# Optimization experiments

Measured on AMD Instinct MI355X. Metric: run time of the kernel, lower is better.

## Reference

```python
import jax, jax.numpy as jnp
import numpy as np

N, T, DYN, STAT, H = 50000, 24, 16, 8, 64
E = 1_600_000


def gru_last(x, Wih, Whh, bih, bhh):
    # x: [N, T, DYN]; torch GRU gate order: r, z, n
    gx = jnp.einsum('ntd,gd->ntg', x, Wih) + bih  # [N, T, 3H]
    h0 = jnp.zeros((x.shape[0], H), x.dtype)

    def step(h, gx_t):
        gh = h @ Whh.T + bhh  # [N, 3H]
        xr, xz, xn = jnp.split(gx_t, 3, axis=-1)
        hr, hz, hn = jnp.split(gh, 3, axis=-1)
        r = jax.nn.sigmoid(xr + hr)
        z = jax.nn.sigmoid(xz + hz)
        n = jnp.tanh(xn + r * hn)
        h_new = (1.0 - z) * n + z * h
        return h_new, None

    h_last, _ = jax.lax.scan(step, h0, jnp.swapaxes(gx, 0, 1))  # scan over T
    return h_last  # [N, H]


def gcn_layer(x, W, b, src, dst, w):
    h = x @ W  # [N, out]
    msg = h[src] * w[:, None]  # gather + weight  [E, out]
    agg = jax.ops.segment_sum(msg, dst, num_segments=N)  # scatter-add
    return agg + b


def setup_inputs() -> dict:
    key = jax.random.key(0)
    ks = jax.random.split(key, 16)
    s = 0.1
    return {
        'x_dyn': jax.random.normal(ks[0], (N, T, DYN), jnp.float32),
        'x_stat': jax.random.normal(ks[1], (N, STAT), jnp.float32),
        'edge_index': jax.random.randint(ks[2], (2, E), 0, N, jnp.int32),
        'edge_weight': jax.random.uniform(ks[3], (E,), jnp.float32),
        'Wih': jax.random.normal(ks[4], (3 * H, DYN), jnp.float32) * s,
        'Whh': jax.random.normal(ks[5], (3 * H, H), jnp.float32) * s,
        'bih': jnp.zeros((3 * H,), jnp.float32),
        'bhh': jnp.zeros((3 * H,), jnp.float32),
        'W1': jax.random.normal(ks[6], (H + STAT, H), jnp.float32) * s,
        'b1': jnp.zeros((H,), jnp.float32),
        'W2': jax.random.normal(ks[7], (H, H), jnp.float32) * s,
        'b2': jnp.zeros((H,), jnp.float32),
        'Wa': jax.random.normal(ks[8], (H, 1), jnp.float32) * s,
        'ba': jnp.zeros((1,), jnp.float32),
        'Wp': jax.random.normal(ks[9], (H, 1), jnp.float32) * s,
        'bp': jnp.zeros((1,), jnp.float32),
    }


def reference(x_dyn, x_stat, edge_index, edge_weight,
              Wih, Whh, bih, bhh, W1, b1, W2, b2, Wa, ba, Wp, bp):
    src, dst = edge_index[0], edge_index[1]
    z = gru_last(x_dyn, Wih, Whh, bih, bhh)            # [N, H]
    h = jnp.concatenate([z, x_stat], axis=1)           # [N, H+STAT]
    h = jax.nn.relu(gcn_layer(h, W1, b1, src, dst, edge_weight))
    h = jax.nn.relu(gcn_layer(h, W2, b2, src, dst, edge_weight))
    # dropout omitted (eval mode)
    aqi = (h @ Wa + ba)[:, 0]
    pm = (h @ Wp + bp)[:, 0]
    return aqi, pm
```

## Files before the change

### kernel.cpp

```cpp
#include <hip/hip_runtime.h>
#include <cstdint>
#include <cstddef>

#define NNODES 50000
#define TT 24
#define DYNF 16
#define STATF 8
#define HDIM 64
#define NEDGES 1600000
#define NB 32
#define GRU_BLOCKS ((NNODES + NB - 1) / NB)
#define FILL_CHUNK 1024
#define FILL_CHUNKS ((NEDGES + FILL_CHUNK - 1) / FILL_CHUNK)
#define CAP 80

typedef __attribute__((ext_vector_type(8))) short bf16x8;
typedef __attribute__((ext_vector_type(4))) float f32x4;
typedef __attribute__((ext_vector_type(2))) float f32x2;

__device__ __forceinline__ unsigned short f2bf(float f) {
    unsigned u = __float_as_uint(f);
    u = (u + 0x7FFFu + ((u >> 16) & 1u)) >> 16;
    return (unsigned short)u;
}
__device__ __forceinline__ float bf2f(unsigned short s) {
    return __uint_as_float((unsigned)s << 16);
}
__device__ __forceinline__ bf16x8 cvt8(const float* __restrict__ p) {
    bf16x8 r;
    #pragma unroll
    for (int i = 0; i < 8; ++i) r[i] = (short)f2bf(p[i]);
    return r;
}
__device__ __forceinline__ bf16x8 zero8() {
    bf16x8 z;
    #pragma unroll
    for (int i = 0; i < 8; ++i) z[i] = 0;
    return z;
}
__device__ __forceinline__ float fast_tanh(float x) {
    float e = __expf(2.f * x);
    return 1.f - 2.f * __builtin_amdgcn_rcpf(e + 1.f);
}

__global__ __launch_bounds__(256, 4) void gru_fill_kernel(
    const float* __restrict__ x_dyn, const float* __restrict__ x_stat,
    const float* __restrict__ Wih, const float* __restrict__ Whh,
    const float* __restrict__ bih, const float* __restrict__ bhh,
    const float* __restrict__ W1, unsigned short* __restrict__ t1,
    const int* __restrict__ srcv, const int* __restrict__ dstv,
    const float* __restrict__ ew, int* __restrict__ cursor,
    unsigned* __restrict__ csr)
{
    constexpr int S_H = 72;
    constexpr int S_X = 40;
    __shared__ short hbuf[2][NB * S_H];
    __shared__ short xbuf[2][NB * S_X];

    const int tid = (int)threadIdx.x;

    if ((int)blockIdx.x >= GRU_BLOCKS) {
        const int fb = (int)blockIdx.x - GRU_BLOCKS;
        const int range = fb & 7;
        const int chunk = fb >> 3;
        const int base = chunk * FILL_CHUNK;
        const int lo = range * (NNODES / 8);
        const int hi = (range == 7) ? NNODES : lo + (NNODES / 8);
        #pragma unroll
        for (int j = 0; j < FILL_CHUNK / 256; ++j) {
            const int e = base + j * 256 + tid;
            if (e < NEDGES) {
                const int d = dstv[e];
                if (d >= lo && d < hi) {
                    const int s = __builtin_nontemporal_load(srcv + e);
                    const float we = __builtin_nontemporal_load(ew + e);
                    const int pos = atomicAdd(&cursor[d], 1);
                    if (pos < CAP)
                        csr[(size_t)d * CAP + pos] =
                            (unsigned)s | ((unsigned)f2bf(we) << 16);
                }
            }
        }
        return;
    }

    const int lane = tid & 63;
    const int w = __builtin_amdgcn_readfirstlane(tid >> 6);
    const int col = lane & 15;
    const int quad = lane >> 4;
    const int node0 = (int)blockIdx.x * NB;

    bf16x8 Bh[3][2];
    bf16x8 Bx[3];
    #pragma unroll
    for (int g = 0; g < 3; ++g) {
        const int n = (w + g * 4) * 16 + col;
        #pragma unroll
        for (int kt = 0; kt < 2; ++kt)
            Bh[g][kt] = cvt8(Whh + (size_t)n * HDIM + kt * 32 + quad * 8);
        Bx[g] = (quad < 2) ? cvt8(Wih + (size_t)n * DYNF + quad * 8) : zero8();
    }

    const int jg = w * 16 + col;
    const float b_r  = bih[jg]        + bhh[jg];
    const float b_z  = bih[HDIM + jg] + bhh[HDIM + jg];
    const float b_xn = bih[2 * HDIM + jg];
    const float b_hn = bhh[2 * HDIM + jg];

    for (int i = tid; i < NB * S_H; i += 256) hbuf[0][i] = 0;

    auto stage_x = [&](int t, int b) {
        const int nd = tid >> 3, c = tid & 7;
        int node = node0 + nd;
        if (node >= NNODES) node = 0;
        const f32x2 v = __builtin_nontemporal_load(
            reinterpret_cast<const f32x2*>(
                x_dyn + (size_t)node * (TT * DYNF) + t * DYNF + c * 2));
        unsigned pk = (unsigned)f2bf(v[0]) | ((unsigned)f2bf(v[1]) << 16);
        *reinterpret_cast<unsigned*>(&xbuf[b][nd * S_X + c * 2]) = pk;
        *reinterpret_cast<unsigned*>(&xbuf[b][nd * S_X + 16 + c * 2]) = 0u;
    };
    stage_x(0, 0);

    float hprev[2][4];
    #pragma unroll
    for (int mt = 0; mt < 2; ++mt)
        #pragma unroll
        for (int r = 0; r < 4; ++r) hprev[mt][r] = 0.f;

    for (int t = 0; t < TT; ++t) {
        const int rb = t & 1;
        __syncthreads();

        f32x4 accr[2], accz[2], accnh[2], accnx[2];
        #pragma unroll
        for (int mt = 0; mt < 2; ++mt) {
            const int nd = mt * 16 + col;
            const bf16x8 a0 = *reinterpret_cast<const bf16x8*>(&hbuf[rb][nd * S_H + quad * 8]);
            const bf16x8 a1 = *reinterpret_cast<const bf16x8*>(&hbuf[rb][nd * S_H + 32 + quad * 8]);
            const bf16x8 ax = *reinterpret_cast<const bf16x8*>(&xbuf[rb][nd * S_X + quad * 8]);
            const f32x4 z4 = {0.f, 0.f, 0.f, 0.f};
            accr[mt]  = __builtin_amdgcn_mfma_f32_16x16x32_bf16(a0, Bh[0][0], z4, 0, 0, 0);
            accr[mt]  = __builtin_amdgcn_mfma_f32_16x16x32_bf16(a1, Bh[0][1], accr[mt], 0, 0, 0);
            accr[mt]  = __builtin_amdgcn_mfma_f32_16x16x32_bf16(ax, Bx[0],    accr[mt], 0, 0, 0);
            accz[mt]  = __builtin_amdgcn_mfma_f32_16x16x32_bf16(a0, Bh[1][0], z4, 0, 0, 0);
            accz[mt]  = __builtin_amdgcn_mfma_f32_16x16x32_bf16(a1, Bh[1][1], accz[mt], 0, 0, 0);
            accz[mt]  = __builtin_amdgcn_mfma_f32_16x16x32_bf16(ax, Bx[1],    accz[mt], 0, 0, 0);
            accnh[mt] = __builtin_amdgcn_mfma_f32_16x16x32_bf16(a0, Bh[2][0], z4, 0, 0, 0);
            accnh[mt] = __builtin_amdgcn_mfma_f32_16x16x32_bf16(a1, Bh[2][1], accnh[mt], 0, 0, 0);
            accnx[mt] = __builtin_amdgcn_mfma_f32_16x16x32_bf16(ax, Bx[2],    z4, 0, 0, 0);
        }

        if (t + 1 < TT) stage_x(t + 1, rb ^ 1);

        #pragma unroll
        for (int mt = 0; mt < 2; ++mt) {
            #pragma unroll
            for (int r = 0; r < 4; ++r) {
                const float dr = 1.f + __expf(-(accr[mt][r] + b_r));
                const float dz = 1.f + __expf(-(accz[mt][r] + b_z));
                const float q  = __builtin_amdgcn_rcpf(dr * dz);
                const float R  = q * dz;
                const float Z  = q * dr;
                const float Nn = fast_tanh(accnx[mt][r] + b_xn + R * (accnh[mt][r] + b_hn));
                const float hn = Nn + Z * (hprev[mt][r] - Nn);
                hprev[mt][r] = hn;
                hbuf[rb ^ 1][(mt * 16 + quad * 4 + r) * S_H + jg] = (short)f2bf(hn);
            }
        }
    }
    __syncthreads();

    bf16x8 Bw0, Bw1, Bw2;
    #pragma unroll
    for (int j = 0; j < 8; ++j) {
        Bw0[j] = (short)f2bf(W1[(size_t)(quad * 8 + j) * HDIM + jg]);
        Bw1[j] = (short)f2bf(W1[(size_t)(32 + quad * 8 + j) * HDIM + jg]);
    }
    if (quad == 0) {
        #pragma unroll
        for (int j = 0; j < 8; ++j)
            Bw2[j] = (short)f2bf(W1[(size_t)(HDIM + j) * HDIM + jg]);
    } else {
        Bw2 = zero8();
    }

    #pragma unroll
    for (int mt = 0; mt < 2; ++mt) {
        const int nd = mt * 16 + col;
        const bf16x8 a0 = *reinterpret_cast<const bf16x8*>(&hbuf[0][nd * S_H + quad * 8]);
        const bf16x8 a1 = *reinterpret_cast<const bf16x8*>(&hbuf[0][nd * S_H + 32 + quad * 8]);
        bf16x8 axs;
        if (quad == 0) {
            int node = node0 + nd;
            if (node >= NNODES) node = 0;
            axs = cvt8(x_stat + (size_t)node * STATF);
        } else {
            axs = zero8();
        }
        const f32x4 z4 = {0.f, 0.f, 0.f, 0.f};
        f32x4 aw;
        aw = __builtin_amdgcn_mfma_f32_16x16x32_bf16(a0, Bw0, z4, 0, 0, 0);
        aw = __builtin_amdgcn_mfma_f32_16x16x32_bf16(a1, Bw1, aw, 0, 0, 0);
        aw = __builtin_amdgcn_mfma_f32_16x16x32_bf16(axs, Bw2, aw, 0, 0, 0);
        #pragma unroll
        for (int r = 0; r < 4; ++r) {
            const int node = node0 + mt * 16 + quad * 4 + r;
            if (node < NNODES) t1[(size_t)node * HDIM + jg] = f2bf(aw[r]);
        }
    }
}

__global__ __launch_bounds__(256) void gather_transform_kernel(
    const unsigned short* __restrict__ tsrc, const int* __restrict__ cursor,
    const unsigned* __restrict__ csr, const float* __restrict__ b1,
    const float* __restrict__ W2, unsigned short* __restrict__ out)
{
    __shared__ float aggL[16][68];
    const int tid  = (int)threadIdx.x;
    const int lane = tid & 63;
    const int w    = tid >> 6;
    const int half = lane >> 5;
    const int fl   = lane & 31;
    const int col  = lane & 15;
    const int quad = lane >> 4;
    const int node0 = (int)blockIdx.x * 16;
    const int jg = w * 16 + col;

    bf16x8 Bw0, Bw1;
    float bk0[8], bk1[8];
    #pragma unroll
    for (int j = 0; j < 8; ++j) {
        Bw0[j] = (short)f2bf(W2[(size_t)(quad * 8 + j) * HDIM + jg]);
        Bw1[j] = (short)f2bf(W2[(size_t)(32 + quad * 8 + j) * HDIM + jg]);
        bk0[j] = b1[quad * 8 + j];
        bk1[j] = b1[32 + quad * 8 + j];
    }

    for (int i = 0; i < 4; ++i) {
        const int nloc = w * 4 + i;
        const int node = node0 + nloc;
        const int beg = node * CAP;
        const int cnt = min(cursor[node], CAP);
        const int end = beg + cnt;
        float ax = 0.f, ay = 0.f;
        int p = beg;
        for (; p + 8 <= end; p += 8) {
            unsigned pp[4], pk[4];
            #pragma unroll
            for (int k = 0; k < 4; ++k) pp[k] = csr[p + 2 * k + half];
            #pragma unroll
            for (int k = 0; k < 4; ++k)
                pk[k] = *reinterpret_cast<const unsigned*>(
                    tsrc + (size_t)(pp[k] & 0xFFFFu) * HDIM + 2 * fl);
            #pragma unroll
            for (int k = 0; k < 4; ++k) {
                const float wgt = __uint_as_float(pp[k] & 0xFFFF0000u);
                ax += wgt * bf2f((unsigned short)(pk[k] & 0xFFFFu));
                ay += wgt * bf2f((unsigned short)(pk[k] >> 16));
            }
        }
        for (; p + 2 <= end; p += 2) {
            const unsigned pp = csr[p + half];
            const unsigned pk = *reinterpret_cast<const unsigned*>(
                tsrc + (size_t)(pp & 0xFFFFu) * HDIM + 2 * fl);
            const float wgt = __uint_as_float(pp & 0xFFFF0000u);
            ax += wgt * bf2f((unsigned short)(pk & 0xFFFFu));
            ay += wgt * bf2f((unsigned short)(pk >> 16));
        }
        if (p < end) {
            const unsigned pp = csr[p];
            const unsigned pk = *reinterpret_cast<const unsigned*>(
                tsrc + (size_t)(pp & 0xFFFFu) * HDIM + 2 * fl);
            const float wgt = (half == 0) ? __uint_as_float(pp & 0xFFFF0000u) : 0.f;
            ax += wgt * bf2f((unsigned short)(pk & 0xFFFFu));
            ay += wgt * bf2f((unsigned short)(pk >> 16));
        }
        ax += __shfl_xor(ax, 32, 64);
        ay += __shfl_xor(ay, 32, 64);
        if (half == 0) {
            f32x2 o; o[0] = ax; o[1] = ay;
            *reinterpret_cast<f32x2*>(&aggL[nloc][2 * fl]) = o;
        }
    }
    __syncthreads();

    bf16x8 a0, a1;
    #pragma unroll
    for (int j = 0; j < 8; ++j) {
        a0[j] = (short)f2bf(fmaxf(aggL[col][quad * 8 + j] + bk0[j], 0.f));
        a1[j] = (short)f2bf(fmaxf(aggL[col][32 + quad * 8 + j] + bk1[j], 0.f));
    }
    const f32x4 z4 = {0.f, 0.f, 0.f, 0.f};
    f32x4 aw;
    aw = __builtin_amdgcn_mfma_f32_16x16x32_bf16(a0, Bw0, z4, 0, 0, 0);
    aw = __builtin_amdgcn_mfma_f32_16x16x32_bf16(a1, Bw1, aw, 0, 0, 0);
    #pragma unroll
    for (int r = 0; r < 4; ++r)
        out[(size_t)(node0 + quad * 4 + r) * HDIM + jg] = f2bf(aw[r]);
}

__global__ __launch_bounds__(256) void gather_head_kernel(
    const unsigned short* __restrict__ tsrc, const int* __restrict__ cursor,
    const unsigned* __restrict__ csr,
    const float* __restrict__ b2, const float* __restrict__ Wa,
    const float* __restrict__ ba, const float* __restrict__ Wp,
    const float* __restrict__ bp, float* __restrict__ out)
{
    const int node = blockIdx.x * 4 + (threadIdx.x >> 6);
    const int lane = (int)threadIdx.x & 63;
    const int half = lane >> 5;
    const int fl = lane & 31;
    if (node >= NNODES) return;
    const int beg = node * CAP;
    const int cnt = min(cursor[node], CAP);
    const int end = beg + cnt;
    float ax = 0.f, ay = 0.f;
    int i = beg;
    for (; i + 8 <= end; i += 8) {
        unsigned p[4], pk[4];
        #pragma unroll
        for (int k = 0; k < 4; ++k) p[k] = csr[i + 2 * k + half];
        #pragma unroll
        for (int k = 0; k < 4; ++k)
            pk[k] = *reinterpret_cast<const unsigned*>(
                tsrc + (size_t)(p[k] & 0xFFFFu) * HDIM + 2 * fl);
        #pragma unroll
        for (int k = 0; k < 4; ++k) {
            const float wgt = __uint_as_float(p[k] & 0xFFFF0000u);
            ax += wgt * bf2f((unsigned short)(pk[k] & 0xFFFFu));
            ay += wgt * bf2f((unsigned short)(pk[k] >> 16));
        }
    }
    for (; i + 2 <= end; i += 2) {
        const unsigned p = csr[i + half];
        const unsigned pk = *reinterpret_cast<const unsigned*>(
            tsrc + (size_t)(p & 0xFFFFu) * HDIM + 2 * fl);
        const float wgt = __uint_as_float(p & 0xFFFF0000u);
        ax += wgt * bf2f((unsigned short)(pk & 0xFFFFu));
        ay += wgt * bf2f((unsigned short)(pk >> 16));
    }
    if (i < end) {
        const unsigned p = csr[i];
        const unsigned pk = *reinterpret_cast<const unsigned*>(
            tsrc + (size_t)(p & 0xFFFFu) * HDIM + 2 * fl);
        const float wgt = (half == 0) ? __uint_as_float(p & 0xFFFF0000u) : 0.f;
        ax += wgt * bf2f((unsigned short)(pk & 0xFFFFu));
        ay += wgt * bf2f((unsigned short)(pk >> 16));
    }
    ax += __shfl_xor(ax, 32, 64);
    ay += __shfl_xor(ay, 32, 64);

    const float2 bb = *reinterpret_cast<const float2*>(b2 + 2 * fl);
    const float2 wa = *reinterpret_cast<const float2*>(Wa + 2 * fl);
    const float2 wp = *reinterpret_cast<const float2*>(Wp + 2 * fl);
    const float h0 = fmaxf(ax + bb.x, 0.f);
    const float h1 = fmaxf(ay + bb.y, 0.f);
    float sa = h0 * wa.x + h1 * wa.y;
    float sp = h0 * wp.x + h1 * wp.y;
    #pragma unroll
    for (int off = 1; off < 32; off <<= 1) {
        sa += __shfl_xor(sa, off, 64);
        sp += __shfl_xor(sp, off, 64);
    }
    if (lane == 0) {
        out[node] = sa + ba[0];
        out[NNODES + node] = sp + bp[0];
    }
}

extern "C" void kernel_launch(void* const* d_in, const int* in_sizes, int n_in,
                              void* d_out, int out_size, void* d_ws, size_t ws_size,
                              hipStream_t stream)
{
    const float* x_dyn  = (const float*)d_in[0];
    const float* x_stat = (const float*)d_in[1];
    const int*   eidx   = (const int*)  d_in[2];
    const float* ew     = (const float*)d_in[3];
    const float* Wih    = (const float*)d_in[4];
    const float* Whh    = (const float*)d_in[5];
    const float* bih    = (const float*)d_in[6];
    const float* bhh    = (const float*)d_in[7];
    const float* W1     = (const float*)d_in[8];
    const float* b1     = (const float*)d_in[9];
    const float* W2     = (const float*)d_in[10];
    const float* b2     = (const float*)d_in[11];
    const float* Wa     = (const float*)d_in[12];
    const float* ba     = (const float*)d_in[13];
    const float* Wp     = (const float*)d_in[14];
    const float* bp     = (const float*)d_in[15];

    const int* srcv = eidx;
    const int* dstv = eidx + NEDGES;

    const size_t NH = (size_t)NNODES * HDIM;
    float* ws   = (float*)d_ws;
    unsigned short* t1 = (unsigned short*)ws;
    unsigned short* t2 = (unsigned short*)(ws + NH / 2);
    unsigned* csr = (unsigned*)(ws + NH);
    int* cursor = (int*)(csr + (size_t)NNODES * CAP);

    dim3 blk(256);

    hipMemsetAsync(cursor, 0, (size_t)NNODES * sizeof(int), stream);

    gru_fill_kernel<<<dim3(GRU_BLOCKS + FILL_CHUNKS * 8), blk, 0, stream>>>(
        x_dyn, x_stat, Wih, Whh, bih, bhh, W1, t1,
        srcv, dstv, ew, cursor, csr);

    gather_transform_kernel<<<dim3(NNODES / 16), blk, 0, stream>>>(
        t1, cursor, csr, b1, W2, t2);

    gather_head_kernel<<<dim3((NNODES + 3) / 4), blk, 0, stream>>>(
        t2, cursor, csr, b2, Wa, ba, Wp, bp, (float*)d_out);
}
```

Measured before the change: 381.7 us.

## Restructure GRU so each wave owns 16 nodes with no block-level barriers

The GRU recurrence is reorganised so each wavefront handles 16 nodes end to end. Weights sit in the MFMA A operand, all 64 hidden features are computed per wave, and the hidden state goes through a private swizzled LDS slice, so the per-timestep __syncthreads is gone. Biases are folded into the input MFMA through a constant-one column, and x is prefetched straight from global into registers. This trades far more register-resident weights (launch bounds lowered to 2) for less barrier and LDS traffic and more independent MFMA work per wave.

```diff
diff --git a/kernel.cpp b/kernel.cpp
--- a/kernel.cpp
+++ b/kernel.cpp
@@ -8,8 +8,7 @@
 #define STATF 8
 #define HDIM 64
 #define NEDGES 1600000
-#define NB 32
-#define GRU_BLOCKS ((NNODES + NB - 1) / NB)
+#define GRUB 782
 #define FILL_CHUNK 1024
 #define FILL_CHUNKS ((NEDGES + FILL_CHUNK - 1) / FILL_CHUNK)
 #define CAP 80
@@ -17,6 +16,7 @@
 typedef __attribute__((ext_vector_type(8))) short bf16x8;
 typedef __attribute__((ext_vector_type(4))) float f32x4;
 typedef __attribute__((ext_vector_type(2))) float f32x2;
+typedef __attribute__((ext_vector_type(2))) unsigned u32x2;
 
 __device__ __forceinline__ unsigned short f2bf(float f) {
     unsigned u = __float_as_uint(f);
@@ -43,7 +43,7 @@
     return 1.f - 2.f * __builtin_amdgcn_rcpf(e + 1.f);
 }
 
-__global__ __launch_bounds__(256, 4) void gru_fill_kernel(
+__global__ __launch_bounds__(256, 2) void gru_fill_kernel(
     const float* __restrict__ x_dyn, const float* __restrict__ x_stat,
     const float* __restrict__ Wih, const float* __restrict__ Whh,
     const float* __restrict__ bih, const float* __restrict__ bhh,
@@ -52,15 +52,12 @@
     const float* __restrict__ ew, int* __restrict__ cursor,
     unsigned* __restrict__ csr)
 {
-    constexpr int S_H = 72;
-    constexpr int S_X = 40;
-    __shared__ short hbuf[2][NB * S_H];
-    __shared__ short xbuf[2][NB * S_X];
+    __shared__ short hsc[4][1024];
 
     const int tid = (int)threadIdx.x;
 
-    if ((int)blockIdx.x >= GRU_BLOCKS) {
-        const int fb = (int)blockIdx.x - GRU_BLOCKS;
+    if ((int)blockIdx.x >= GRUB) {
+        const int fb = (int)blockIdx.x - GRUB;
         const int range = fb & 7;
         const int chunk = fb >> 3;
         const int base = chunk * FILL_CHUNK;
@@ -85,129 +82,163 @@
     }
 
     const int lane = tid & 63;
-    const int w = __builtin_amdgcn_readfirstlane(tid >> 6);
+    const int wv = tid >> 6;
     const int col = lane & 15;
     const int quad = lane >> 4;
-    const int node0 = (int)blockIdx.x * NB;
-
-    bf16x8 Bh[3][2];
-    bf16x8 Bx[3];
+
+    int node0 = (int)blockIdx.x * 64 + wv * 16;
+    const bool active = node0 < NNODES;
+    if (!active) node0 = 0;
+
+    bf16x8 Wh[3][4][2];
+    bf16x8 Wx[3][4];
     #pragma unroll
     for (int g = 0; g < 3; ++g) {
-        const int n = (w + g * 4) * 16 + col;
-        #pragma unroll
-        for (int kt = 0; kt < 2; ++kt)
-            Bh[g][kt] = cvt8(Whh + (size_t)n * HDIM + kt * 32 + quad * 8);
-        Bx[g] = (quad < 2) ? cvt8(Wih + (size_t)n * DYNF + quad * 8) : zero8();
-    }
-
-    const int jg = w * 16 + col;
-    const float b_r  = bih[jg]        + bhh[jg];
-    const float b_z  = bih[HDIM + jg] + bhh[HDIM + jg];
-    const float b_xn = bih[2 * HDIM + jg];
-    const float b_hn = bhh[2 * HDIM + jg];
-
-    for (int i = tid; i < NB * S_H; i += 256) hbuf[0][i] = 0;
-
-    auto stage_x = [&](int t, int b) {
-        const int nd = tid >> 3, c = tid & 7;
-        int node = node0 + nd;
-        if (node >= NNODES) node = 0;
-        const f32x2 v = __builtin_nontemporal_load(
-            reinterpret_cast<const f32x2*>(
-                x_dyn + (size_t)node * (TT * DYNF) + t * DYNF + c * 2));
-        unsigned pk = (unsigned)f2bf(v[0]) | ((unsigned)f2bf(v[1]) << 16);
-        *reinterpret_cast<unsigned*>(&xbuf[b][nd * S_X + c * 2]) = pk;
-        *reinterpret_cast<unsigned*>(&xbuf[b][nd * S_X + 16 + c * 2]) = 0u;
+        #pragma unroll
+        for (int ft = 0; ft < 4; ++ft) {
+            const int row = g * 64 + ft * 16 + col;
+            Wh[g][ft][0] = cvt8(Whh + (size_t)row * HDIM + quad * 8);
+            Wh[g][ft][1] = cvt8(Whh + (size_t)row * HDIM + 32 + quad * 8);
+            if (quad < 2) {
+                Wx[g][ft] = cvt8(Wih + (size_t)row * DYNF + quad * 8);
+            } else {
+                bf16x8 z = zero8();
+                if (quad == 2) {
+                    const float bias = bih[row] + ((g < 2) ? bhh[row] : 0.f);
+                    z[0] = (short)f2bf(bias);
+                }
+                Wx[g][ft] = z;
+            }
+        }
+    }
+    float bhn[4][4];
+    #pragma unroll
+    for (int ft = 0; ft < 4; ++ft)
+        #pragma unroll
+        for (int r = 0; r < 4; ++r)
+            bhn[ft][r] = bhh[128 + ft * 16 + quad * 4 + r];
+
+    short* hs = &hsc[wv][0];
+    const int wsw = (col & 7) << 3;
+
+    auto xload = [&](int t, f32x4& lo, f32x4& hi) {
+        if (quad < 2) {
+            const float* p = x_dyn + (size_t)(node0 + col) * (TT * DYNF)
+                           + t * DYNF + quad * 8;
+            lo = *reinterpret_cast<const f32x4*>(p);
+            hi = *reinterpret_cast<const f32x4*>(p + 4);
+        }
     };
-    stage_x(0, 0);
-
-    float hprev[2][4];
-    #pragma unroll
-    for (int mt = 0; mt < 2; ++mt)
-        #pragma unroll
-        for (int r = 0; r < 4; ++r) hprev[mt][r] = 0.f;
+    auto xcvt = [&](f32x4 lo, f32x4 hi) -> bf16x8 {
+        bf16x8 b;
+        if (quad < 2) {
+            #pragma unroll
+            for (int i = 0; i < 4; ++i) {
+                b[i] = (short)f2bf(lo[i]);
+                b[4 + i] = (short)f2bf(hi[i]);
+            }
+        } else {
+            b = zero8();
+            if (quad == 2) b[0] = (short)0x3F80;
+        }
+        return b;
+    };
+
+    f32x4 xlo, xhi;
+    xload(0, xlo, xhi);
+    bf16x8 Bh0 = zero8(), Bh1 = zero8();
+    bf16x8 Bx = xcvt(xlo, xhi);
+
+    float hprev[4][4];
+    #pragma unroll
+    for (int ft = 0; ft < 4; ++ft)
+        #pragma unroll
+        for (int r = 0; r < 4; ++r) hprev[ft][r] = 0.f;
+
+    const f32x4 z4 = {0.f, 0.f, 0.f, 0.f};
 
     for (int t = 0; t < TT; ++t) {
-        const int rb = t & 1;
-        __syncthreads();
-
-        f32x4 accr[2], accz[2], accnh[2], accnx[2];
-        #pragma unroll
-        for (int mt = 0; mt < 2; ++mt) {
-            const int nd = mt * 16 + col;
-            const bf16x8 a0 = *reinterpret_cast<const bf16x8*>(&hbuf[rb][nd * S_H + quad * 8]);
-            const bf16x8 a1 = *reinterpret_cast<const bf16x8*>(&hbuf[rb][nd * S_H + 32 + quad * 8]);
-            const bf16x8 ax = *reinterpret_cast<const bf16x8*>(&xbuf[rb][nd * S_X + quad * 8]);
-            const f32x4 z4 = {0.f, 0.f, 0.f, 0.f};
-            accr[mt]  = __builtin_amdgcn_mfma_f32_16x16x32_bf16(a0, Bh[0][0], z4, 0, 0, 0);
-            accr[mt]  = __builtin_amdgcn_mfma_f32_16x16x32_bf16(a1, Bh[0][1], accr[mt], 0, 0, 0);
-            accr[mt]  = __builtin_amdgcn_mfma_f32_16x16x32_bf16(ax, Bx[0],    accr[mt], 0, 0, 0);
-            accz[mt]  = __builtin_amdgcn_mfma_f32_16x16x32_bf16(a0, Bh[1][0], z4, 0, 0, 0);
-            accz[mt]  = __builtin_amdgcn_mfma_f32_16x16x32_bf16(a1, Bh[1][1], accz[mt], 0, 0, 0);
-            accz[mt]  = __builtin_amdgcn_mfma_f32_16x16x32_bf16(ax, Bx[1],    accz[mt], 0, 0, 0);
-            accnh[mt] = __builtin_amdgcn_mfma_f32_16x16x32_bf16(a0, Bh[2][0], z4, 0, 0, 0);
-            accnh[mt] = __builtin_amdgcn_mfma_f32_16x16x32_bf16(a1, Bh[2][1], accnh[mt], 0, 0, 0);
-            accnx[mt] = __builtin_amdgcn_mfma_f32_16x16x32_bf16(ax, Bx[2],    z4, 0, 0, 0);
-        }
-
-        if (t + 1 < TT) stage_x(t + 1, rb ^ 1);
-
-        #pragma unroll
-        for (int mt = 0; mt < 2; ++mt) {
+        f32x4 nlo, nhi;
+        if (t + 1 < TT) xload(t + 1, nlo, nhi);
+
+        #pragma unroll
+        for (int ft = 0; ft < 4; ++ft) {
+            f32x4 ar, az, anh, anx;
+            ar  = __builtin_amdgcn_mfma_f32_16x16x32_bf16(Wh[0][ft][0], Bh0, z4, 0, 0, 0);
+            ar  = __builtin_amdgcn_mfma_f32_16x16x32_bf16(Wh[0][ft][1], Bh1, ar, 0, 0, 0);
+            ar  = __builtin_amdgcn_mfma_f32_16x16x32_bf16(Wx[0][ft],    Bx,  ar, 0, 0, 0);
+            az  = __builtin_amdgcn_mfma_f32_16x16x32_bf16(Wh[1][ft][0], Bh0, z4, 0, 0, 0);
+            az  = __builtin_amdgcn_mfma_f32_16x16x32_bf16(Wh[1][ft][1], Bh1, az, 0, 0, 0);
+            az  = __builtin_amdgcn_mfma_f32_16x16x32_bf16(Wx[1][ft],    Bx,  az, 0, 0, 0);
+            anh = __builtin_amdgcn_mfma_f32_16x16x32_bf16(Wh[2][ft][0], Bh0, z4, 0, 0, 0);
+            anh = __builtin_amdgcn_mfma_f32_16x16x32_bf16(Wh[2][ft][1], Bh1, anh, 0, 0, 0);
+            anx = __builtin_amdgcn_mfma_f32_16x16x32_bf16(Wx[2][ft],    Bx,  z4, 0, 0, 0);
+
+            unsigned plo, phi;
             #pragma unroll
             for (int r = 0; r < 4; ++r) {
-                const float dr = 1.f + __expf(-(accr[mt][r] + b_r));
-                const float dz = 1.f + __expf(-(accz[mt][r] + b_z));
+                const float dr = 1.f + __expf(-ar[r]);
+                const float dz = 1.f + __expf(-az[r]);
                 const float q  = __builtin_amdgcn_rcpf(dr * dz);
                 const float R  = q * dz;
                 const float Z  = q * dr;
-                const float Nn = fast_tanh(accnx[mt][r] + b_xn + R * (accnh[mt][r] + b_hn));
-                const float hn = Nn + Z * (hprev[mt][r] - Nn);
-                hprev[mt][r] = hn;
-                hbuf[rb ^ 1][(mt * 16 + quad * 4 + r) * S_H + jg] = (short)f2bf(hn);
+                const float Nn = fast_tanh(anx[r] + R * (anh[r] + bhn[ft][r]));
+                const float hn = Nn + Z * (hprev[ft][r] - Nn);
+                hprev[ft][r] = hn;
+                const unsigned hb = f2bf(hn);
+                if (r == 0) plo = hb;
+                else if (r == 1) plo |= hb << 16;
+                else if (r == 2) phi = hb;
+                else phi |= hb << 16;
             }
-        }
-    }
-    __syncthreads();
-
-    bf16x8 Bw0, Bw1, Bw2;
-    #pragma unroll
-    for (int j = 0; j < 8; ++j) {
-        Bw0[j] = (short)f2bf(W1[(size_t)(quad * 8 + j) * HDIM + jg]);
-        Bw1[j] = (short)f2bf(W1[(size_t)(32 + quad * 8 + j) * HDIM + jg]);
-    }
-    if (quad == 0) {
-        #pragma unroll
-        for (int j = 0; j < 8; ++j)
-            Bw2[j] = (short)f2bf(W1[(size_t)(HDIM + j) * HDIM + jg]);
-    } else {
-        Bw2 = zero8();
-    }
-
-    #pragma unroll
-    for (int mt = 0; mt < 2; ++mt) {
-        const int nd = mt * 16 + col;
-        const bf16x8 a0 = *reinterpret_cast<const bf16x8*>(&hbuf[0][nd * S_H + quad * 8]);
-        const bf16x8 a1 = *reinterpret_cast<const bf16x8*>(&hbuf[0][nd * S_H + 32 + quad * 8]);
-        bf16x8 axs;
+            u32x2 pk; pk[0] = plo; pk[1] = phi;
+            *reinterpret_cast<u32x2*>(
+                &hs[col * 64 + ((ft * 16 + quad * 4) ^ wsw)]) = pk;
+        }
+
+        Bh0 = *reinterpret_cast<const bf16x8*>(&hs[col * 64 + ((quad * 8) ^ wsw)]);
+        Bh1 = *reinterpret_cast<const bf16x8*>(&hs[col * 64 + ((32 + quad * 8) ^ wsw)]);
+        if (t + 1 < TT) Bx = xcvt(nlo, nhi);
+    }
+
+    if (!active) return;
+
+    bf16x8 Aw[4][2];
+    #pragma unroll
+    for (int ot = 0; ot < 4; ++ot)
+        #pragma unroll
+        for (int kt = 0; kt < 2; ++kt)
+            #pragma unroll
+            for (int j = 0; j < 8; ++j)
+                Aw[ot][kt][j] = (short)f2bf(
+                    W1[(size_t)(kt * 32 + quad * 8 + j) * HDIM + ot * 16 + col]);
+    bf16x8 Aw2[4];
+    #pragma unroll
+    for (int ot = 0; ot < 4; ++ot) {
         if (quad == 0) {
-            int node = node0 + nd;
-            if (node >= NNODES) node = 0;
-            axs = cvt8(x_stat + (size_t)node * STATF);
+            #pragma unroll
+            for (int j = 0; j < 8; ++j)
+                Aw2[ot][j] = (short)f2bf(
+                    W1[(size_t)(HDIM + j) * HDIM + ot * 16 + col]);
         } else {
-            axs = zero8();
-        }
-        const f32x4 z4 = {0.f, 0.f, 0.f, 0.f};
+            Aw2[ot] = zero8();
+        }
+    }
+    bf16x8 Bxs;
+    if (quad == 0) Bxs = cvt8(x_stat + (size_t)(node0 + col) * STATF);
+    else Bxs = zero8();
+
+    #pragma unroll
+    for (int ot = 0; ot < 4; ++ot) {
         f32x4 aw;
-        aw = __builtin_amdgcn_mfma_f32_16x16x32_bf16(a0, Bw0, z4, 0, 0, 0);
-        aw = __builtin_amdgcn_mfma_f32_16x16x32_bf16(a1, Bw1, aw, 0, 0, 0);
-        aw = __builtin_amdgcn_mfma_f32_16x16x32_bf16(axs, Bw2, aw, 0, 0, 0);
-        #pragma unroll
-        for (int r = 0; r < 4; ++r) {
-            const int node = node0 + mt * 16 + quad * 4 + r;
-            if (node < NNODES) t1[(size_t)node * HDIM + jg] = f2bf(aw[r]);
-        }
+        aw = __builtin_amdgcn_mfma_f32_16x16x32_bf16(Aw[ot][0], Bh0, z4, 0, 0, 0);
+        aw = __builtin_amdgcn_mfma_f32_16x16x32_bf16(Aw[ot][1], Bh1, aw, 0, 0, 0);
+        aw = __builtin_amdgcn_mfma_f32_16x16x32_bf16(Aw2[ot],   Bxs, aw, 0, 0, 0);
+        u32x2 pk;
+        pk[0] = (unsigned)f2bf(aw[0]) | ((unsigned)f2bf(aw[1]) << 16);
+        pk[1] = (unsigned)f2bf(aw[2]) | ((unsigned)f2bf(aw[3]) << 16);
+        *reinterpret_cast<u32x2*>(
+            &t1[(size_t)(node0 + col) * HDIM + ot * 16 + quad * 4]) = pk;
     }
 }
 
@@ -404,7 +435,7 @@
 
     hipMemsetAsync(cursor, 0, (size_t)NNODES * sizeof(int), stream);
 
-    gru_fill_kernel<<<dim3(GRU_BLOCKS + FILL_CHUNKS * 8), blk, 0, stream>>>(
+    gru_fill_kernel<<<dim3(GRUB + FILL_CHUNKS * 8), blk, 0, stream>>>(
         x_dyn, x_stat, Wih, Whh, bih, bhh, W1, t1,
         srcv, dstv, ew, cursor, csr);
 
```

After: 502.3 us. +31.6%, slower.
